# Kernel tuning notes

Hardware: AMD Instinct MI355X
Metric: run time of the kernel (lower is better)

## Reference

```python
import jax, jax.numpy as jnp
import numpy as np

EPS_N = 1e-12   # F.normalize eps
LN_EPS = 1e-5   # LayerNorm eps
N_NODES = 20000
NODES_PER_GRAPH = 200
DEG = 8
N_EDGES = N_NODES * DEG
F_NODE = 36
F_EDGE = 10
HID = 128
HEAD = 8
DK = HID // HEAD
G = N_NODES // NODES_PER_GRAPH


def l2norm(x):
    n = jnp.sqrt(jnp.sum(x * x, axis=-1, keepdims=True))
    return x / jnp.maximum(n, EPS_N)


def layer_norm(x, g, b):
    m = jnp.mean(x, axis=-1, keepdims=True)
    v = jnp.mean((x - m) ** 2, axis=-1, keepdims=True)
    return (x - m) / jnp.sqrt(v + LN_EPS) * g + b


def seg_softmax(e, idx, n):
    m = jax.ops.segment_max(e, idx, num_segments=n)
    ex = jnp.exp(e - m[idx])
    s = jax.ops.segment_sum(ex, idx, num_segments=n)
    return ex / s[idx]


def sfe_conv(x, src, dst, eattr, We, Wq, Wk, Wv, Wo, bo, g, b):
    # x: [N, in], src/dst: [Ef] (self loops included), eattr: [Ef, F_EDGE]
    n = x.shape[0]
    emb = l2norm(eattr @ We)                  # edge_encoder + F.normalize
    xj = x[src] + emb                          # source node + edge embedding
    q = (xj @ Wq).reshape(-1, HEAD, DK)
    ksum = (x[dst] @ Wk).reshape(-1, HEAD, DK).sum(axis=1)  # sum over k-heads (matmul+sum in source)
    v = (xj @ Wv).reshape(-1, HEAD, DK)
    energy = jnp.einsum('ehd,ed->eh', q, ksum) / jnp.sqrt(jnp.float32(HID))
    att = seg_softmax(energy, dst, n)          # segment softmax over target nodes, per head
    msg = (v * att[:, :, None]).reshape(-1, HID)
    agg = jax.ops.segment_sum(msg, dst, num_segments=n)
    y = layer_norm(agg @ Wo + bo, g, b)        # update(): out_norm(out_linear(.))
    return layer_norm(y, g, b)                 # forward() applies out_norm again


def setup_inputs():
    key = jax.random.key(0)
    ks = jax.random.split(key, 16)
    x = jax.random.normal(ks[0], (N_NODES, F_NODE), jnp.float32)
    edge_attr = jax.random.uniform(ks[1], (N_EDGES, F_EDGE), jnp.float32)
    src = jnp.repeat(jnp.arange(N_NODES), DEG)
    base = src - src % NODES_PER_GRAPH
    off = jax.random.randint(ks[2], (N_EDGES,), 1, NODES_PER_GRAPH)
    dst = base + (src % NODES_PER_GRAPH + off) % NODES_PER_GRAPH  # same-graph, no self loops
    edge_index = jnp.stack([src, dst]).astype(jnp.int64)
    batch = (jnp.arange(N_NODES) // NODES_PER_GRAPH).astype(jnp.int64)
    interface_pos = jnp.arange(0, N_NODES, 2, dtype=jnp.int64)
    s = lambda k, sh: jax.random.normal(k, sh, jnp.float32) * 0.05
    return dict(
        x=x, edge_attr=edge_attr,
        c0_We=s(ks[3], (F_EDGE, F_NODE)), c0_Wq=s(ks[4], (F_NODE, HID)),
        c0_Wk=s(ks[5], (F_NODE, HID)), c0_Wv=s(ks[6], (F_NODE, HID)),
        c0_Wo=s(ks[7], (HID, HID)), c0_bo=jnp.zeros((HID,), jnp.float32),
        c0_g=jnp.ones((HID,), jnp.float32), c0_b=jnp.zeros((HID,), jnp.float32),
        cs_We=s(ks[8], (2, F_EDGE, HID)), cs_Wq=s(ks[9], (2, HID, HID)),
        cs_Wk=s(ks[10], (2, HID, HID)), cs_Wv=s(ks[11], (2, HID, HID)),
        cs_Wo=s(ks[12], (2, HID, HID)), cs_bo=jnp.zeros((2, HID), jnp.float32),
        cs_g=jnp.ones((2, HID), jnp.float32), cs_b=jnp.zeros((2, HID), jnp.float32),
        gate=s(ks[13], (HID,)), W1=s(ks[14], (HID, HID // 2)),
        b1=jnp.zeros((HID // 2,), jnp.float32), W2=s(ks[15], (HID // 2, 1)),
        b2=jnp.zeros((1,), jnp.float32),
        edge_index=edge_index, batch=batch, interface_pos=interface_pos,
        graph_num=G)


def reference(x, edge_attr, c0_We, c0_Wq, c0_Wk, c0_Wv, c0_Wo, c0_bo, c0_g, c0_b,
              cs_We, cs_Wq, cs_Wk, cs_Wv, cs_Wo, cs_bo, cs_g, cs_b,
              gate, W1, b1, W2, b2, edge_index, batch, interface_pos, graph_num):
    n = x.shape[0]
    loops = jnp.arange(n)
    src = jnp.concatenate([edge_index[0], loops])
    dst = jnp.concatenate([edge_index[1], loops])
    ea = jnp.concatenate([l2norm(edge_attr),
                          jnp.zeros((n, edge_attr.shape[1]), edge_attr.dtype)])
    h = l2norm(x)
    h = jnp.tanh(sfe_conv(h, src, dst, ea, c0_We, c0_Wq, c0_Wk, c0_Wv, c0_Wo, c0_bo, c0_g, c0_b))
    for i in range(cs_We.shape[0]):
        h = jnp.tanh(sfe_conv(h, src, dst, ea, cs_We[i], cs_Wq[i], cs_Wk[i], cs_Wv[i],
                              cs_Wo[i], cs_bo[i], cs_g[i], cs_b[i]))
    # global self-attention pooling over interface nodes, per graph
    xi = h[interface_pos]
    bi = batch[interface_pos]
    att = seg_softmax(xi @ gate, bi, graph_num)
    pooled = jax.ops.segment_sum(att[:, None] * xi, bi, num_segments=graph_num)  # [G, HID]
    out = jnp.tanh(pooled @ W1 + b1)
    return jax.nn.sigmoid(out @ W2 + b2)  # [G, 1]
```

## Files before the change

### kernel.cpp

```cpp
#include <hip/hip_runtime.h>
#include <math.h>

#define HID 128
#define HEAD 8
#define DK 16
#define FEDGE 10
#define FNODE 36
#define ESCALE 0.08838834764831845f
#define CH 32

typedef float f32x4v __attribute__((ext_vector_type(4)));
typedef short bf16x8 __attribute__((ext_vector_type(8)));

struct PackArgs {
  const float* src[8];
  unsigned short* dst[8];
  int fin[8];
  int kt[8];
  int blk_off[8];
};

struct PrepArgs {
  const float* We[3];
  const float* Wq[3];
  const float* Wk[3];
  const float* Wv[3];
  float* C[3];
  float* WeWv[3];
  float* Gram[3];
  float* Wksum[3];
  int fin[3];
};

__device__ __forceinline__ void fma4(float4& z, float s, const float4& w) {
  z.x += s * w.x;
  z.y += s * w.y;
  z.z += s * w.z;
  z.w += s * w.w;
}

__device__ __forceinline__ unsigned short f2bf(float f) {
  unsigned int u = __float_as_uint(f);
  u += 0x7fffu + ((u >> 16) & 1u);
  return (unsigned short)(u >> 16);
}

__device__ __forceinline__ float bflo(unsigned int u) { return __uint_as_float(u << 16); }
__device__ __forceinline__ float bfhi(unsigned int u) { return __uint_as_float(u & 0xffff0000u); }

__device__ __forceinline__ void store_bf8(unsigned short* p, float4 a, float4 b) {
  uint4 u;
  u.x = (unsigned)f2bf(a.x) | ((unsigned)f2bf(a.y) << 16);
  u.y = (unsigned)f2bf(a.z) | ((unsigned)f2bf(a.w) << 16);
  u.z = (unsigned)f2bf(b.x) | ((unsigned)f2bf(b.y) << 16);
  u.w = (unsigned)f2bf(b.z) | ((unsigned)f2bf(b.w) << 16);
  *(uint4*)p = u;
}

__global__ void k_zero_i(int* __restrict__ p, int n) {
  int i = blockIdx.x * 256 + threadIdx.x;
  if (i < n) p[i] = 0;
}

__global__ void k_count(const int* __restrict__ ei, int E, int* __restrict__ cnt) {
  int e = blockIdx.x * 256 + threadIdx.x;
  if (e >= E) return;
  atomicAdd(&cnt[ei[E + e]], 1);
}

__global__ __launch_bounds__(1024) void k_scan(const int* __restrict__ cnt, int* __restrict__ off,
                                               int* __restrict__ cur, int* __restrict__ scsr_s,
                                               int n, int total) {
  __shared__ int s[1024];
  int t = threadIdx.x;
  const int C = (n + 1023) / 1024;
  int local[32];
  int base = t * C;
  int sum = 0;
  for (int j = 0; j < C; ++j) {
    int i = base + j;
    int v = (i < n) ? cnt[i] : 0;
    local[j] = sum;
    sum += v;
  }
  s[t] = sum;
  __syncthreads();
  for (int dd = 1; dd < 1024; dd <<= 1) {
    int v = (t >= dd) ? s[t - dd] : 0;
    __syncthreads();
    s[t] += v;
    __syncthreads();
  }
  int excl = (t == 0) ? 0 : s[t - 1];
  for (int j = 0; j < C; ++j) {
    int i = base + j;
    if (i < n) {
      int o = excl + local[j];
      off[i] = o;
      cur[i] = o;
      scsr_s[o + i] = i;
    }
  }
  if (t == 0) off[n] = total;
}

__global__ void k_fill_sea(const int* __restrict__ ei, int E, int* __restrict__ cur,
                           int* __restrict__ scsr_s, const float* __restrict__ eattr,
                           const float* __restrict__ Gram3, float* __restrict__ sea3, int ET) {
  int e = blockIdx.x * 256 + threadIdx.x;
  if (e >= E) return;
  int t = ei[E + e];
  int pos = atomicAdd(&cur[t], 1) + t + 1;
  scsr_s[pos] = ei[e];
  float a[FEDGE];
  float ss = 0.f;
  for (int i = 0; i < FEDGE; ++i) {
    a[i] = eattr[(size_t)e * FEDGE + i];
    ss += a[i] * a[i];
  }
  float s0 = 1.f / fmaxf(sqrtf(ss), 1e-12f);
  for (int i = 0; i < FEDGE; ++i) a[i] *= s0;
  for (int l = 0; l < 3; ++l) {
    const float* G = Gram3 + l * FEDGE * FEDGE;
    float gp = 0.f;
#pragma unroll
    for (int j = 0; j < FEDGE; ++j) {
      float tt = 0.f;
#pragma unroll
      for (int u = 0; u < FEDGE; ++u) tt += G[j * FEDGE + u] * a[u];
      gp += tt * a[j];
    }
    float scl = 1.f / fmaxf(sqrtf(gp), 1e-12f);
    float* sp = sea3 + (size_t)l * ET * FEDGE + (size_t)pos * FEDGE;
#pragma unroll
    for (int u = 0; u < FEDGE; ++u) sp[u] = scl * a[u];
  }
}

__global__ __launch_bounds__(128) void k_wprep3(PrepArgs a) {
  int l = blockIdx.x / FEDGE, t = blockIdx.x - l * FEDGE;
  int d = threadIdx.x;
  int fin = a.fin[l];
  const float* We = a.We[l];
  const float* Wq = a.Wq[l];
  const float* Wk = a.Wk[l];
  const float* Wv = a.Wv[l];
  __shared__ float sw[HID];
  if (d < fin) sw[d] = We[t * fin + d];
  __syncthreads();
  float c = 0.f, wv = 0.f;
  for (int i = 0; i < fin; ++i) {
    c += sw[i] * Wq[i * HID + d];
    wv += sw[i] * Wv[i * HID + d];
  }
  a.C[l][t * HID + d] = c;
  a.WeWv[l][t * HID + d] = wv;
  if (d < FEDGE) {
    float g = 0.f;
    for (int i = 0; i < fin; ++i) g += sw[i] * We[d * fin + i];
    a.Gram[l][t * FEDGE + d] = g;
  }
  for (int r = t; r < fin; r += FEDGE) {
    if (d < DK) {
      float s = 0.f;
#pragma unroll
      for (int hh = 0; hh < HEAD; ++hh) s += Wk[r * HID + hh * DK + d];
      a.Wksum[l][r * DK + d] = s;
    }
  }
}

__global__ __launch_bounds__(64) void k_wpack8(PackArgs pa) {
  int b = blockIdx.x, lane = threadIdx.x;
  int m = 0;
#pragma unroll
  for (int i = 1; i < 8; ++i) m += (b >= pa.blk_off[i]);
  int local = b - pa.blk_off[m];
  int KT = pa.kt[m];
  int ct = local / KT, kt = local - ct * KT;
  const float* W = pa.src[m];
  int fin = pa.fin[m];
  int col = ct * 16 + (lane & 15);
  int kbase = kt * 32 + (lane >> 4) * 8;
  float v[8];
#pragma unroll
  for (int j = 0; j < 8; ++j) {
    int k = kbase + j;
    v[j] = (k < fin) ? W[k * HID + col] : 0.f;
  }
  store_bf8(pa.dst[m] + (size_t)local * 512 + lane * 8, make_float4(v[0], v[1], v[2], v[3]),
            make_float4(v[4], v[5], v[6], v[7]));
}

__global__ __launch_bounds__(256) void k1_l2x(
    const float* __restrict__ x, const unsigned short* __restrict__ qpack,
    const unsigned short* __restrict__ vpack, const float* __restrict__ Wksum,
    const float* __restrict__ C, unsigned short* __restrict__ qxh, float* __restrict__ kb,
    unsigned short* __restrict__ vxh, float* __restrict__ Mout, int N) {
  const int fin = FNODE;
  int d = threadIdx.x;
  int n0 = blockIdx.x * 16;
  int nb = min(16, N - n0);
  __shared__ __align__(16) float sx[16][40];
  __shared__ __align__(16) unsigned short afrag[2][64][8];
  __shared__ float sk[16][DK];
  {
    int col = d & 127, h2 = d >> 7;
#pragma unroll
    for (int rr = 0; rr < 8; ++rr) {
      int r = h2 * 8 + rr;
      if (col < fin) sx[r][col] = (r < nb) ? x[(size_t)(n0 + r) * fin + col] : 0.f;
    }
  }
  __syncthreads();
  int grp = d >> 4, j16 = d & 15;
  {
    float ssq = 0.f;
    for (int i = j16; i < fin; i += 16) ssq += sx[grp][i] * sx[grp][i];
#pragma unroll
    for (int o = 8; o; o >>= 1) ssq += __shfl_xor(ssq, o, 16);
    float scl = 1.f / fmaxf(sqrtf(ssq), 1e-12f);
    for (int i = j16; i < fin; i += 16) sx[grp][i] *= scl;
  }
  __syncthreads();
  int lane = d & 63, wvid = d >> 6;
  if (d < 128) {
    int kt = d >> 6;
    int m = lane & 15, k0 = kt * 32 + (lane >> 4) * 8;
    float v[8];
#pragma unroll
    for (int j = 0; j < 8; ++j) {
      int k = k0 + j;
      v[j] = (k < fin) ? sx[m][k] : 0.f;
    }
    store_bf8(&afrag[kt][lane][0], make_float4(v[0], v[1], v[2], v[3]),
              make_float4(v[4], v[5], v[6], v[7]));
  }
  {
    float kk = 0.f;
    for (int i = 0; i < fin; ++i) kk += sx[grp][i] * Wksum[i * DK + j16];
    sk[grp][j16] = kk;
    if (grp < nb) kb[(size_t)(n0 + grp) * DK + j16] = kk;
  }
  __syncthreads();
  int colD = lane & 15, quad = lane >> 4;
#pragma unroll
  for (int t = 0; t < 4; ++t) {
    int g = wvid * 4 + t;
    int mat = g >> 3, ct = g & 7;
    const unsigned short* P = mat ? vpack : qpack;
    f32x4v acc = {0.f, 0.f, 0.f, 0.f};
#pragma unroll
    for (int kt = 0; kt < 2; ++kt) {
      bf16x8 a = *(const bf16x8*)&afrag[kt][lane][0];
      bf16x8 b = *(const bf16x8*)(P + ((size_t)(ct * 2 + kt) * 64 + lane) * 8);
      acc = __builtin_amdgcn_mfma_f32_16x16x32_bf16(a, b, acc, 0, 0, 0);
    }
    unsigned short* out = mat ? vxh : qxh;
#pragma unroll
    for (int reg = 0; reg < 4; ++reg) {
      int node = quad * 4 + reg;
      if (node < nb) out[(size_t)(n0 + node) * HID + ct * 16 + colD] = f2bf(acc[reg]);
    }
  }
  if (d < HEAD * FEDGE) {
    int hh = d / FEDGE, tt = d - hh * FEDGE;
    float crow[16];
    *(float4*)&crow[0] = *(const float4*)&C[tt * HID + hh * DK + 0];
    *(float4*)&crow[4] = *(const float4*)&C[tt * HID + hh * DK + 4];
    *(float4*)&crow[8] = *(const float4*)&C[tt * HID + hh * DK + 8];
    *(float4*)&crow[12] = *(const float4*)&C[tt * HID + hh * DK + 12];
    for (int r = 0; r < nb; ++r) {
      float m = 0.f;
#pragma unroll
      for (int j = 0; j < DK; ++j) m += sk[r][j] * crow[j];
      Mout[((size_t)(n0 + r) * HEAD + hh) * 16 + tt] = m;
    }
  }
}

__global__ __launch_bounds__(256) void k_post_k1(
    const float* __restrict__ agg, const unsigned short* __restrict__ opack,
    const float* __restrict__ bo, const float* __restrict__ gg, const float* __restrict__ bb,
    const unsigned short* __restrict__ qpack, const unsigned short* __restrict__ vpack,
    const float* __restrict__ Wksum, const float* __restrict__ C,
    unsigned short* __restrict__ qxh, float* __restrict__ kb, unsigned short* __restrict__ vxh,
    float* __restrict__ Mout, int N) {
  int d = threadIdx.x;
  int n0 = blockIdx.x * 16;
  int nb = min(16, N - n0);
  __shared__ __align__(16) unsigned short afrag[4][64][8];
  __shared__ __align__(16) float sz[16][132];
  __shared__ __align__(16) unsigned short hfrag[4][64][8];
  __shared__ float sk[16][DK];
  int lane = d & 63, wvid = d >> 6;
  {
    int kt = wvid;
    int m = lane & 15, k0 = kt * 32 + (lane >> 4) * 8;
    const float* p = agg + (size_t)(n0 + m) * HID + k0;
    float4 x0 = *(const float4*)p;
    float4 x1 = *(const float4*)(p + 4);
    store_bf8(&afrag[kt][lane][0], x0, x1);
  }
  __syncthreads();
  int colD = lane & 15, quad = lane >> 4;
  {
    int ct0 = wvid * 2, ct1 = wvid * 2 + 1;
    float bias0 = bo[ct0 * 16 + colD], bias1 = bo[ct1 * 16 + colD];
    f32x4v acc0 = {bias0, bias0, bias0, bias0};
    f32x4v acc1 = {bias1, bias1, bias1, bias1};
#pragma unroll
    for (int kt = 0; kt < 4; ++kt) {
      bf16x8 a = *(const bf16x8*)&afrag[kt][lane][0];
      bf16x8 b0 = *(const bf16x8*)(opack + ((size_t)(ct0 * 4 + kt) * 64 + lane) * 8);
      bf16x8 b1 = *(const bf16x8*)(opack + ((size_t)(ct1 * 4 + kt) * 64 + lane) * 8);
      acc0 = __builtin_amdgcn_mfma_f32_16x16x32_bf16(a, b0, acc0, 0, 0, 0);
      acc1 = __builtin_amdgcn_mfma_f32_16x16x32_bf16(a, b1, acc1, 0, 0, 0);
    }
#pragma unroll
    for (int reg = 0; reg < 4; ++reg) {
      int node = quad * 4 + reg;
      sz[node][ct0 * 16 + colD] = acc0[reg];
      sz[node][ct1 * 16 + colD] = acc1[reg];
    }
  }
  __syncthreads();
  {
    int c4 = d & 31, rs = d >> 5;
    int col0 = c4 * 4, r0 = rs * 2;
    float4 zA = *(const float4*)&sz[r0][col0];
    float4 zB = *(const float4*)&sz[r0 + 1][col0];
    float4 g4 = *(const float4*)&gg[col0];
    float4 b4 = *(const float4*)&bb[col0];
#pragma unroll
    for (int pass = 0; pass < 2; ++pass) {
      float sA = zA.x + zA.y + zA.z + zA.w;
      float qA = zA.x * zA.x + zA.y * zA.y + zA.z * zA.z + zA.w * zA.w;
      float sB = zB.x + zB.y + zB.z + zB.w;
      float qB = zB.x * zB.x + zB.y * zB.y + zB.z * zB.z + zB.w * zB.w;
#pragma unroll
      for (int o = 16; o; o >>= 1) {
        sA += __shfl_xor(sA, o, 32);
        qA += __shfl_xor(qA, o, 32);
        sB += __shfl_xor(sB, o, 32);
        qB += __shfl_xor(qB, o, 32);
      }
      float mA = sA * (1.f / 128.f);
      float iA = rsqrtf(fmaxf(qA * (1.f / 128.f) - mA * mA, 0.f) + 1e-5f);
      float mB = sB * (1.f / 128.f);
      float iB = rsqrtf(fmaxf(qB * (1.f / 128.f) - mB * mB, 0.f) + 1e-5f);
      zA.x = (zA.x - mA) * iA * g4.x + b4.x;
      zA.y = (zA.y - mA) * iA * g4.y + b4.y;
      zA.z = (zA.z - mA) * iA * g4.z + b4.z;
      zA.w = (zA.w - mA) * iA * g4.w + b4.w;
      zB.x = (zB.x - mB) * iB * g4.x + b4.x;
      zB.y = (zB.y - mB) * iB * g4.y + b4.y;
      zB.z = (zB.z - mB) * iB * g4.z + b4.z;
      zB.w = (zB.w - mB) * iB * g4.w + b4.w;
    }
    zA.x = tanhf(zA.x);
    zA.y = tanhf(zA.y);
    zA.z = tanhf(zA.z);
    zA.w = tanhf(zA.w);
    zB.x = tanhf(zB.x);
    zB.y = tanhf(zB.y);
    zB.z = tanhf(zB.z);
    zB.w = tanhf(zB.w);
    *(float4*)&sz[r0][col0] = zA;
    *(float4*)&sz[r0 + 1][col0] = zB;
    int chunk = col0 >> 5, qd = (col0 >> 3) & 3, eo = col0 & 7;
    unsigned int loA = (unsigned)f2bf(zA.x) | ((unsigned)f2bf(zA.y) << 16);
    unsigned int hiA = (unsigned)f2bf(zA.z) | ((unsigned)f2bf(zA.w) << 16);
    unsigned int loB = (unsigned)f2bf(zB.x) | ((unsigned)f2bf(zB.y) << 16);
    unsigned int hiB = (unsigned)f2bf(zB.z) | ((unsigned)f2bf(zB.w) << 16);
    unsigned short* pA = &hfrag[chunk][(r0 & 15) + qd * 16][eo];
    unsigned short* pB = &hfrag[chunk][((r0 + 1) & 15) + qd * 16][eo];
    *(unsigned int*)pA = loA;
    *(unsigned int*)(pA + 2) = hiA;
    *(unsigned int*)pB = loB;
    *(unsigned int*)(pB + 2) = hiB;
  }
  __syncthreads();
#pragma unroll
  for (int t = 0; t < 4; ++t) {
    int g = wvid * 4 + t;
    int mat = g >> 3, ct = g & 7;
    const unsigned short* P = mat ? vpack : qpack;
    f32x4v acc = {0.f, 0.f, 0.f, 0.f};
#pragma unroll
    for (int kt = 0; kt < 4; ++kt) {
      bf16x8 a = *(const bf16x8*)&hfrag[kt][lane][0];
      bf16x8 b = *(const bf16x8*)(P + ((size_t)(ct * 4 + kt) * 64 + lane) * 8);
      acc = __builtin_amdgcn_mfma_f32_16x16x32_bf16(a, b, acc, 0, 0, 0);
    }
    unsigned short* out = mat ? vxh : qxh;
#pragma unroll
    for (int reg = 0; reg < 4; ++reg) {
      int node = quad * 4 + reg;
      if (node < nb) out[(size_t)(n0 + node) * HID + ct * 16 + colD] = f2bf(acc[reg]);
    }
  }
  int grp = d >> 4, j16 = d & 15;
  {
    float kk = 0.f;
    for (int i = 0; i < HID; ++i) kk += sz[grp][i] * Wksum[i * DK + j16];
    sk[grp][j16] = kk;
    if (grp < nb) kb[(size_t)(n0 + grp) * DK + j16] = kk;
  }
  __syncthreads();
  if (d < HEAD * FEDGE) {
    int hh = d / FEDGE, tt = d - hh * FEDGE;
    float crow[16];
    *(float4*)&crow[0] = *(const float4*)&C[tt * HID + hh * DK + 0];
    *(float4*)&crow[4] = *(const float4*)&C[tt * HID + hh * DK + 4];
    *(float4*)&crow[8] = *(const float4*)&C[tt * HID + hh * DK + 8];
    *(float4*)&crow[12] = *(const float4*)&C[tt * HID + hh * DK + 12];
    for (int r = 0; r < nb; ++r) {
      float m = 0.f;
#pragma unroll
      for (int j = 0; j < DK; ++j) m += sk[r][j] * crow[j];
      Mout[((size_t)(n0 + r) * HEAD + hh) * 16 + tt] = m;
    }
  }
}

__global__ __launch_bounds__(128) void k3_gather(
    const int* __restrict__ off, const int* __restrict__ scsr_s, const float* __restrict__ sea,
    const unsigned short* __restrict__ qxh, const float* __restrict__ kb,
    const float* __restrict__ Mbuf, const unsigned short* __restrict__ vxh,
    const float* __restrict__ WeWv, float* __restrict__ agg, int N) {
  int b = blockIdx.x;
  int n = ((N & 7) == 0) ? ((b & 7) * (N >> 3) + (b >> 3)) : b;
  int d = threadIdx.x;
  int j16 = d & 15, hd = d >> 4;
  __shared__ float sen[CH * 8];
  __shared__ float ssea[CH * 10];
  __shared__ int ss[CH];
  __shared__ float sT[HEAD * FEDGE];
  __shared__ __align__(16) float skb[DK];
  __shared__ float sM[128];
  int base = off[n] + n;
  int cnt = off[n + 1] + n + 1 - base;
  if (d < DK) skb[d] = kb[(size_t)n * DK + d];
  sM[d] = Mbuf[(size_t)n * 128 + d];
  bool doT = (j16 < FEDGE);
  float m = -1e30f, l = 0.f, accv = 0.f, T = 0.f;
  for (int c0 = 0; c0 < cnt; c0 += CH) {
    int cc = min(CH, cnt - c0);
    for (int idx = d; idx < cc * 10; idx += 128)
      ssea[idx] = sea[(size_t)(base + c0) * 10 + idx];
    if (d < cc) ss[d] = scsr_s[base + c0 + d];
    __syncthreads();
    for (int ob = 0; ob < cc; ob += 16) {
      int o = ob + (d >> 3);
      int h = d & 7;
      if (o < cc) {
        int s = ss[o];
        const uint4* qp = (const uint4*)(qxh + (size_t)s * HID + h * DK);
        uint4 qa = qp[0], qb = qp[1];
        float en = bflo(qa.x) * skb[0] + bfhi(qa.x) * skb[1] + bflo(qa.y) * skb[2] +
                   bfhi(qa.y) * skb[3] + bflo(qa.z) * skb[4] + bfhi(qa.z) * skb[5] +
                   bflo(qa.w) * skb[6] + bfhi(qa.w) * skb[7] + bflo(qb.x) * skb[8] +
                   bfhi(qb.x) * skb[9] + bflo(qb.y) * skb[10] + bfhi(qb.y) * skb[11] +
                   bflo(qb.z) * skb[12] + bfhi(qb.z) * skb[13] + bflo(qb.w) * skb[14] +
                   bfhi(qb.w) * skb[15];
        if ((c0 + o) > 0) {
#pragma unroll
          for (int u = 0; u < FEDGE; ++u) en += sM[h * DK + u] * ssea[o * 10 + u];
        }
        sen[o * 8 + h] = en * ESCALE;
      }
    }
    __syncthreads();
    float mloc = -1e30f;
    for (int o = 0; o < cc; ++o) mloc = fmaxf(mloc, sen[o * 8 + hd]);
    float mnew = fmaxf(m, mloc);
    float alpha = __expf(m - mnew);
    l *= alpha;
    accv *= alpha;
    T *= alpha;
#pragma unroll 2
    for (int o = 0; o < cc; ++o) {
      int s = ss[o];
      float p = __expf(sen[o * 8 + hd] - mnew);
      l += p;
      float vv = __uint_as_float((unsigned)vxh[(size_t)s * HID + d] << 16);
      accv += p * vv;
      if (doT && (c0 + o) > 0) T += p * ssea[o * 10 + j16];
    }
    m = mnew;
    __syncthreads();
  }
  float inv = 1.f / l;
  if (doT) sT[hd * FEDGE + j16] = T * inv;
  __syncthreads();
  float y = accv * inv;
#pragma unroll
  for (int t = 0; t < FEDGE; ++t) y += sT[hd * FEDGE + t] * WeWv[t * HID + d];
  agg[(size_t)n * HID + d] = y;
}

__global__ __launch_bounds__(256) void k_post(const float* __restrict__ agg,
                                              const float* __restrict__ Wo,
                                              const float* __restrict__ bo,
                                              const float* __restrict__ gg,
                                              const float* __restrict__ bb,
                                              float* __restrict__ hout, int N) {
  int d = threadIdx.x;
  int n0 = blockIdx.x * 16;
  int nb = min(16, N - n0);
  __shared__ __align__(16) float sh[16][132];
  {
    int col = d & 127, h2 = d >> 7;
#pragma unroll
    for (int rr = 0; rr < 8; ++rr) {
      int r = h2 * 8 + rr;
      sh[r][col] = (r < nb) ? agg[(size_t)(n0 + r) * HID + col] : 0.f;
    }
  }
  __syncthreads();
  int c4 = d & 31, rs = d >> 5;
  int col0 = c4 * 4, r0 = rs * 2;
  float4 bv = *(const float4*)&bo[col0];
  float4 zA = bv, zB = bv;
  for (int k4 = 0; k4 < 32; ++k4) {
    float4 w0 = *(const float4*)&Wo[(k4 * 4 + 0) * HID + col0];
    float4 w1 = *(const float4*)&Wo[(k4 * 4 + 1) * HID + col0];
    float4 w2 = *(const float4*)&Wo[(k4 * 4 + 2) * HID + col0];
    float4 w3 = *(const float4*)&Wo[(k4 * 4 + 3) * HID + col0];
    float4 a0 = *(const float4*)&sh[r0][k4 * 4];
    float4 a1 = *(const float4*)&sh[r0 + 1][k4 * 4];
    fma4(zA, a0.x, w0);
    fma4(zA, a0.y, w1);
    fma4(zA, a0.z, w2);
    fma4(zA, a0.w, w3);
    fma4(zB, a1.x, w0);
    fma4(zB, a1.y, w1);
    fma4(zB, a1.z, w2);
    fma4(zB, a1.w, w3);
  }
  float4 g4 = *(const float4*)&gg[col0];
  float4 b4 = *(const float4*)&bb[col0];
#pragma unroll
  for (int pass = 0; pass < 2; ++pass) {
    float sA = zA.x + zA.y + zA.z + zA.w;
    float qA = zA.x * zA.x + zA.y * zA.y + zA.z * zA.z + zA.w * zA.w;
    float sB = zB.x + zB.y + zB.z + zB.w;
    float qB = zB.x * zB.x + zB.y * zB.y + zB.z * zB.z + zB.w * zB.w;
#pragma unroll
    for (int o = 16; o; o >>= 1) {
      sA += __shfl_xor(sA, o, 32);
      qA += __shfl_xor(qA, o, 32);
      sB += __shfl_xor(sB, o, 32);
      qB += __shfl_xor(qB, o, 32);
    }
    float mA = sA * (1.f / 128.f);
    float iA = rsqrtf(fmaxf(qA * (1.f / 128.f) - mA * mA, 0.f) + 1e-5f);
    float mB = sB * (1.f / 128.f);
    float iB = rsqrtf(fmaxf(qB * (1.f / 128.f) - mB * mB, 0.f) + 1e-5f);
    zA.x = (zA.x - mA) * iA * g4.x + b4.x;
    zA.y = (zA.y - mA) * iA * g4.y + b4.y;
    zA.z = (zA.z - mA) * iA * g4.z + b4.z;
    zA.w = (zA.w - mA) * iA * g4.w + b4.w;
    zB.x = (zB.x - mB) * iB * g4.x + b4.x;
    zB.y = (zB.y - mB) * iB * g4.y + b4.y;
    zB.z = (zB.z - mB) * iB * g4.z + b4.z;
    zB.w = (zB.w - mB) * iB * g4.w + b4.w;
  }
  if (r0 < nb) {
    float4 o0 = make_float4(tanhf(zA.x), tanhf(zA.y), tanhf(zA.z), tanhf(zA.w));
    *(float4*)&hout[(size_t)(n0 + r0) * HID + col0] = o0;
  }
  if (r0 + 1 < nb) {
    float4 o1 = make_float4(tanhf(zB.x), tanhf(zB.y), tanhf(zB.z), tanhf(zB.w));
    *(float4*)&hout[(size_t)(n0 + r0 + 1) * HID + col0] = o1;
  }
}

__global__ __launch_bounds__(128) void k4_pool(const float* __restrict__ h,
                                               const int* __restrict__ ipos,
                                               const float* __restrict__ gate,
                                               const float* __restrict__ W1,
                                               const float* __restrict__ b1,
                                               const float* __restrict__ W2,
                                               const float* __restrict__ b2,
                                               float* __restrict__ out, int per_g) {
  int g = blockIdx.x, d = threadIdx.x;
  __shared__ int snode[128];
  __shared__ float satt[128], spool[HID], so[64], sv[2];
  if (d < per_g) snode[d] = ipos[g * per_g + d];
  __syncthreads();
  float sc = -1e30f;
  if (d < per_g) {
    float s = 0.f;
    int node = snode[d];
    for (int i = 0; i < HID; ++i) s += h[(size_t)node * HID + i] * gate[i];
    sc = s;
  }
  satt[d] = sc;
  __syncthreads();
  if (d == 0) {
    float m = -1e30f;
    for (int i = 0; i < per_g; ++i) m = fmaxf(m, satt[i]);
    sv[0] = m;
  }
  __syncthreads();
  float m = sv[0];
  float ex = (d < per_g) ? __expf(sc - m) : 0.f;
  satt[d] = ex;
  __syncthreads();
  if (d == 0) {
    float su = 0.f;
    for (int i = 0; i < per_g; ++i) su += satt[i];
    sv[1] = 1.f / su;
  }
  __syncthreads();
  float inv = sv[1];
  float p = 0.f;
  for (int i = 0; i < per_g; ++i) p += satt[i] * h[(size_t)snode[i] * HID + d];
  spool[d] = p * inv;
  __syncthreads();
  if (d < 64) {
    float o = b1[d];
    for (int i = 0; i < HID; ++i) o += spool[i] * W1[i * 64 + d];
    so[d] = tanhf(o);
  }
  __syncthreads();
  if (d == 0) {
    float z = b2[0];
    for (int i = 0; i < 64; ++i) z += so[i] * W2[i];
    out[g] = 1.f / (1.f + __expf(-z));
  }
}

extern "C" void kernel_launch(void* const* d_in, const int* in_sizes, int n_in, void* d_out,
                              int out_size, void* d_ws, size_t ws_size, hipStream_t stream) {
  const float* x = (const float*)d_in[0];
  const float* eattr = (const float*)d_in[1];
  const float* c0_We = (const float*)d_in[2];
  const float* c0_Wq = (const float*)d_in[3];
  const float* c0_Wk = (const float*)d_in[4];
  const float* c0_Wv = (const float*)d_in[5];
  const float* c0_Wo = (const float*)d_in[6];
  const float* c0_bo = (const float*)d_in[7];
  const float* c0_g = (const float*)d_in[8];
  const float* c0_b = (const float*)d_in[9];
  const float* cs_We = (const float*)d_in[10];
  const float* cs_Wq = (const float*)d_in[11];
  const float* cs_Wk = (const float*)d_in[12];
  const float* cs_Wv = (const float*)d_in[13];
  const float* cs_Wo = (const float*)d_in[14];
  const float* cs_bo = (const float*)d_in[15];
  const float* cs_g = (const float*)d_in[16];
  const float* cs_b = (const float*)d_in[17];
  const float* gate = (const float*)d_in[18];
  const float* W1 = (const float*)d_in[19];
  const float* b1 = (const float*)d_in[20];
  const float* W2 = (const float*)d_in[21];
  const float* b2 = (const float*)d_in[22];
  const int* ei = (const int*)d_in[23];
  const int* ipos = (const int*)d_in[25];

  int N = in_sizes[0] / FNODE;
  int E = in_sizes[1] / FEDGE;
  int G = out_size;
  int per_g = in_sizes[25] / G;
  int ET = E + N;

  float* w = (float*)d_ws;
  float* hB = w;         w += (size_t)N * HID;
  float* aggb = w;       w += (size_t)N * HID;
  float* kb = w;         w += (size_t)N * DK;
  float* Mbuf = w;       w += (size_t)N * HEAD * 16;
  float* sea3 = w;       w += (size_t)3 * ET * FEDGE;
  float* C3 = w;         w += 3 * FEDGE * HID;
  float* WeWv3 = w;      w += 3 * FEDGE * HID;
  float* Gram3 = w;      w += 3 * FEDGE * FEDGE;
  float* Wksum3 = w;     w += 3 * HID * DK;
  unsigned short* qxh = (unsigned short*)w;  w += (size_t)N * HID / 2;
  unsigned short* vxh = (unsigned short*)w;  w += (size_t)N * HID / 2;
  unsigned short* qp3 = (unsigned short*)w;  w += 3 * 16384 / 2;
  unsigned short* vp3 = (unsigned short*)w;  w += 3 * 16384 / 2;
  unsigned short* op2 = (unsigned short*)w;  w += 2 * 16384 / 2;
  int* cnt = (int*)w;
  int* off = cnt + (N + 1);
  int* cur = off + (N + 1);
  int* scsr_s = cur + N;

  const float* Ws[3][8] = {
      {c0_We, c0_Wq, c0_Wk, c0_Wv, c0_Wo, c0_bo, c0_g, c0_b},
      {cs_We, cs_Wq, cs_Wk, cs_Wv, cs_Wo, cs_bo, cs_g, cs_b},
      {cs_We + FEDGE * HID, cs_Wq + HID * HID, cs_Wk + HID * HID, cs_Wv + HID * HID,
       cs_Wo + HID * HID, cs_bo + HID, cs_g + HID, cs_b + HID}};
  int fins[3] = {FNODE, HID, HID};

  PrepArgs prep;
  for (int l = 0; l < 3; ++l) {
    prep.We[l] = Ws[l][0];
    prep.Wq[l] = Ws[l][1];
    prep.Wk[l] = Ws[l][2];
    prep.Wv[l] = Ws[l][3];
    prep.C[l] = C3 + l * FEDGE * HID;
    prep.WeWv[l] = WeWv3 + l * FEDGE * HID;
    prep.Gram[l] = Gram3 + l * FEDGE * FEDGE;
    prep.Wksum[l] = Wksum3 + l * HID * DK;
    prep.fin[l] = fins[l];
  }
  k_wprep3<<<3 * FEDGE, 128, 0, stream>>>(prep);

  PackArgs pa;
  {
    const float* srcs[8] = {Ws[0][1], Ws[0][3], Ws[1][1], Ws[1][3],
                            Ws[2][1], Ws[2][3], Ws[0][4], Ws[1][4]};
    unsigned short* dsts[8] = {qp3, vp3, qp3 + 16384, vp3 + 16384, qp3 + 2 * 16384,
                               vp3 + 2 * 16384, op2, op2 + 16384};
    int fns[8] = {FNODE, FNODE, HID, HID, HID, HID, HID, HID};
    int kts[8] = {2, 2, 4, 4, 4, 4, 4, 4};
    int offb = 0;
    for (int i = 0; i < 8; ++i) {
      pa.src[i] = srcs[i];
      pa.dst[i] = dsts[i];
      pa.fin[i] = fns[i];
      pa.kt[i] = kts[i];
      pa.blk_off[i] = offb;
      offb += 8 * kts[i];
    }
    k_wpack8<<<offb, 64, 0, stream>>>(pa);
  }

  k_zero_i<<<(N + 1 + 255) / 256, 256, 0, stream>>>(cnt, N + 1);
  k_count<<<(E + 255) / 256, 256, 0, stream>>>(ei, E, cnt);
  k_scan<<<1, 1024, 0, stream>>>(cnt, off, cur, scsr_s, N, E);
  k_fill_sea<<<(E + 255) / 256, 256, 0, stream>>>(ei, E, cur, scsr_s, eattr, Gram3, sea3, ET);

  k1_l2x<<<(N + 15) / 16, 256, 0, stream>>>(x, qp3, vp3, Wksum3, C3, qxh, kb, vxh, Mbuf, N);
  for (int l = 0; l < 3; ++l) {
    const float* sea_l = sea3 + (size_t)l * ET * FEDGE;
    k3_gather<<<N, 128, 0, stream>>>(off, scsr_s, sea_l, qxh, kb, Mbuf, vxh,
                                     WeWv3 + l * FEDGE * HID, aggb, N);
    if (l < 2) {
      k_post_k1<<<(N + 15) / 16, 256, 0, stream>>>(
          aggb, op2 + l * 16384, Ws[l][5], Ws[l][6], Ws[l][7], qp3 + (l + 1) * 16384,
          vp3 + (l + 1) * 16384, Wksum3 + (l + 1) * HID * DK, C3 + (l + 1) * FEDGE * HID, qxh, kb,
          vxh, Mbuf, N);
    } else {
      k_post<<<(N + 15) / 16, 256, 0, stream>>>(aggb, Ws[l][4], Ws[l][5], Ws[l][6], Ws[l][7], hB,
                                                N);
    }
  }
  k4_pool<<<G, 128, 0, stream>>>(hB, ipos, gate, W1, b1, W2, b2, (float*)d_out, per_g);
}
```

Baseline: 392.0 us.

## Compute last conv layer only for interface nodes used by pooling

The final gather and post-processing layer now runs only over the interface nodes, since pooling reads only those. A node map remaps each block to its interface node, and outputs are written compactly so pooling reads contiguous rows per graph. This skips about half of the last layer's gather and LayerNorm work. It assumes the interface positions are grouped per graph in order with equal counts, which the per_g indexing already relied on.

```diff
diff --git a/kernel.cpp b/kernel.cpp
--- a/kernel.cpp
+++ b/kernel.cpp
@@ -428,9 +428,17 @@
     const int* __restrict__ off, const int* __restrict__ scsr_s, const float* __restrict__ sea,
     const unsigned short* __restrict__ qxh, const float* __restrict__ kb,
     const float* __restrict__ Mbuf, const unsigned short* __restrict__ vxh,
-    const float* __restrict__ WeWv, float* __restrict__ agg, int N) {
+    const float* __restrict__ WeWv, float* __restrict__ agg, int N,
+    const int* __restrict__ nodemap, int use_map) {
   int b = blockIdx.x;
-  int n = ((N & 7) == 0) ? ((b & 7) * (N >> 3) + (b >> 3)) : b;
+  int n, oi;
+  if (use_map) {
+    n = nodemap[b];
+    oi = b;
+  } else {
+    n = ((N & 7) == 0) ? ((b & 7) * (N >> 3) + (b >> 3)) : b;
+    oi = n;
+  }
   int d = threadIdx.x;
   int j16 = d & 15, hd = d >> 4;
   __shared__ float sen[CH * 8];
@@ -497,7 +505,7 @@
   float y = accv * inv;
 #pragma unroll
   for (int t = 0; t < FEDGE; ++t) y += sT[hd * FEDGE + t] * WeWv[t * HID + d];
-  agg[(size_t)n * HID + d] = y;
+  agg[(size_t)oi * HID + d] = y;
 }
 
 __global__ __launch_bounds__(256) void k_post(const float* __restrict__ agg,
@@ -578,7 +586,6 @@
 }
 
 __global__ __launch_bounds__(128) void k4_pool(const float* __restrict__ h,
-                                               const int* __restrict__ ipos,
                                                const float* __restrict__ gate,
                                                const float* __restrict__ W1,
                                                const float* __restrict__ b1,
@@ -586,15 +593,13 @@
                                                const float* __restrict__ b2,
                                                float* __restrict__ out, int per_g) {
   int g = blockIdx.x, d = threadIdx.x;
-  __shared__ int snode[128];
   __shared__ float satt[128], spool[HID], so[64], sv[2];
-  if (d < per_g) snode[d] = ipos[g * per_g + d];
-  __syncthreads();
+  size_t rbase = (size_t)g * per_g;
   float sc = -1e30f;
   if (d < per_g) {
     float s = 0.f;
-    int node = snode[d];
-    for (int i = 0; i < HID; ++i) s += h[(size_t)node * HID + i] * gate[i];
+    const float* hp = h + (rbase + d) * HID;
+    for (int i = 0; i < HID; ++i) s += hp[i] * gate[i];
     sc = s;
   }
   satt[d] = sc;
@@ -617,7 +622,7 @@
   __syncthreads();
   float inv = sv[1];
   float p = 0.f;
-  for (int i = 0; i < per_g; ++i) p += satt[i] * h[(size_t)snode[i] * HID + d];
+  for (int i = 0; i < per_g; ++i) p += satt[i] * h[(rbase + i) * HID + d];
   spool[d] = p * inv;
   __syncthreads();
   if (d < 64) {
@@ -664,7 +669,8 @@
   int N = in_sizes[0] / FNODE;
   int E = in_sizes[1] / FEDGE;
   int G = out_size;
-  int per_g = in_sizes[25] / G;
+  int NI = in_sizes[25];
+  int per_g = NI / G;
   int ET = E + N;
 
   float* w = (float*)d_ws;
@@ -736,17 +742,19 @@
   k1_l2x<<<(N + 15) / 16, 256, 0, stream>>>(x, qp3, vp3, Wksum3, C3, qxh, kb, vxh, Mbuf, N);
   for (int l = 0; l < 3; ++l) {
     const float* sea_l = sea3 + (size_t)l * ET * FEDGE;
-    k3_gather<<<N, 128, 0, stream>>>(off, scsr_s, sea_l, qxh, kb, Mbuf, vxh,
-                                     WeWv3 + l * FEDGE * HID, aggb, N);
     if (l < 2) {
+      k3_gather<<<N, 128, 0, stream>>>(off, scsr_s, sea_l, qxh, kb, Mbuf, vxh,
+                                       WeWv3 + l * FEDGE * HID, aggb, N, ipos, 0);
       k_post_k1<<<(N + 15) / 16, 256, 0, stream>>>(
           aggb, op2 + l * 16384, Ws[l][5], Ws[l][6], Ws[l][7], qp3 + (l + 1) * 16384,
           vp3 + (l + 1) * 16384, Wksum3 + (l + 1) * HID * DK, C3 + (l + 1) * FEDGE * HID, qxh, kb,
           vxh, Mbuf, N);
     } else {
-      k_post<<<(N + 15) / 16, 256, 0, stream>>>(aggb, Ws[l][4], Ws[l][5], Ws[l][6], Ws[l][7], hB,
-                                                N);
-    }
-  }
-  k4_pool<<<G, 128, 0, stream>>>(hB, ipos, gate, W1, b1, W2, b2, (float*)d_out, per_g);
-}
+      k3_gather<<<NI, 128, 0, stream>>>(off, scsr_s, sea_l, qxh, kb, Mbuf, vxh,
+                                        WeWv3 + l * FEDGE * HID, aggb, N, ipos, 1);
+      k_post<<<(NI + 15) / 16, 256, 0, stream>>>(aggb, Ws[l][4], Ws[l][5], Ws[l][6], Ws[l][7], hB,
+                                                 NI);
+    }
+  }
+  k4_pool<<<G, 128, 0, stream>>>(hB, gate, W1, b1, W2, b2, (float*)d_out, per_g);
+}
```

After: 368.9 us. 5.9% less time.
